# Optimization experiments

Measured on AMD Instinct MI355X. Metric: run time of the kernel, lower is better.

The kernel has to match this reference:

```python
import jax, jax.numpy as jnp
import numpy as np

R = 8          # shuffle_rate
HEADS = 4
DIM_HEAD = 64


def setup_inputs() -> dict:
    key = jax.random.key(0)
    k1, k2, k3 = jax.random.split(key, 3)
    dim = 64
    C = dim * R * R            # 4096, token channel dim after unshuffle
    inner = HEADS * DIM_HEAD   # 256
    x = jax.random.normal(k1, (8, dim, 256, 256), dtype=jnp.float32)
    W_qkv = jax.random.normal(k2, (C, 3 * inner), dtype=jnp.float32) * (C ** -0.5)
    W_out = jax.random.normal(k3, (inner, C), dtype=jnp.float32) * (inner ** -0.5)
    b_out = jnp.zeros((C,), dtype=jnp.float32)
    return {"x": x, "W_qkv": W_qkv, "W_out": W_out, "b_out": b_out}


def reference(x, W_qkv, W_out, b_out):
    scale = DIM_HEAD ** -0.5
    B, C0, H0, W0 = x.shape
    h, w = H0 // R, W0 // R
    N = h * w
    C = C0 * R * R
    # PixelUnshuffle: [B,C0,H0,W0] -> [B, C0*R*R, h, w]
    xd = x.reshape(B, C0, h, R, w, R).transpose(0, 1, 3, 5, 2, 4).reshape(B, C, h, w)
    # flatten spatial -> tokens [B, N, C]
    tokens = xd.reshape(B, C, N).transpose(0, 2, 1)
    qkv = tokens @ W_qkv                                   # [B, N, 3*inner]
    q, k, v = jnp.split(qkv, 3, axis=-1)
    def heads(t):  # [B,N,inner] -> [B,H,N,d]
        return t.reshape(B, N, HEADS, DIM_HEAD).transpose(0, 2, 1, 3)
    q, k, v = heads(q), heads(k), heads(v)
    dots = jnp.einsum('bhnd,bhmd->bhnm', q, k) * scale
    attn = jax.nn.softmax(dots, axis=-1)
    out = jnp.einsum('bhnm,bhmd->bhnd', attn, v)
    out = out.transpose(0, 2, 1, 3).reshape(B, N, HEADS * DIM_HEAD)
    y = out @ W_out + b_out                                # [B, N, C]
    y = y.transpose(0, 2, 1).reshape(B, C, h, w)
    # PixelShuffle: [B, C0*R*R, h, w] -> [B, C0, H0, W0]
    y = y.reshape(B, C0, R, R, h, w).transpose(0, 1, 4, 2, 5, 3).reshape(B, C0, H0, W0)
    return y
```

## Files before the change

kernel.cpp:

```cpp
#include <hip/hip_runtime.h>

typedef unsigned short u16;
typedef __attribute__((ext_vector_type(8))) short s16x8;
typedef __attribute__((ext_vector_type(4))) short s16x4;
typedef __attribute__((ext_vector_type(4))) float f32x4;

__device__ __forceinline__ u16 f2bf(float f) {
    unsigned int u;
    __builtin_memcpy(&u, &f, 4);
    unsigned int r = u + 0x7FFFu + ((u >> 16) & 1u);
    return (u16)(r >> 16);
}

__device__ __forceinline__ unsigned int cvt_pk_bf16(float a, float b) {
    unsigned int r;
    asm("v_cvt_pk_bf16_f32 %0, %1, %2" : "=v"(r) : "v"(a), "v"(b));
    return r;
}

__device__ __forceinline__ void gl_lds16(const u16* g, u16* l) {
    __builtin_amdgcn_global_load_lds(
        (const __attribute__((address_space(1))) unsigned int*)g,
        (__attribute__((address_space(3))) unsigned int*)l,
        16, 0, 0);
}

__global__ __launch_bounds__(256) void k_transpose(const float* __restrict__ in,
                                                   u16* __restrict__ out,
                                                   int rows, int cols) {
    __shared__ float tile[64][65];
    int bx = blockIdx.x * 64, by = blockIdx.y * 64;
    int tx = threadIdx.x & 63, ty = threadIdx.x >> 6;
    for (int i = ty; i < 64; i += 4)
        tile[i][tx] = in[(size_t)(by + i) * cols + bx + tx];
    __syncthreads();
    for (int i = ty; i < 64; i += 4)
        out[(size_t)(bx + i) * rows + by + tx] = f2bf(tile[tx][i]);
}

__global__ __launch_bounds__(512, 1) void k_gemm_qkv(const float* __restrict__ x,
                                                     const u16* __restrict__ Bt,
                                                     float* __restrict__ P) {
    const int K = 4096;
    __shared__ u16 As[256 * 64];
    __shared__ u16 Bs[256 * 64];
    const int tid = threadIdx.x;
    const int wave = tid >> 6, lane = tid & 63;
    const int quad = lane >> 4, l15 = lane & 15;
    const int wm = wave >> 2, wn = wave & 3;

    int lin = blockIdx.x;
    int rem = (lin & 7) * 48 + (lin >> 3);
    int tn3 = rem % 3;
    int q   = rem / 3;
    int z   = q >> 5;
    int tmi = q & 31;
    const int tm = tmi * 256, tn = tn3 * 256;

    const int b   = tm >> 10;
    const int yy0 = (tm & 1023) >> 5;
    const float* asrc = x + ((size_t)(b * 64 + z * 16)) * 65536
                          + yy0 * 2048 + tid * 4;

    u16* dstA[8];
#pragma unroll
    for (int seg = 0; seg < 8; ++seg) {
        int xx  = (tid >> 1) & 31;
        int row = seg * 32 + xx;
        int k2  = wave * 16 + (tid & 1) * 8;
        int byteoff = (row * 128 + k2) ^ ((row & 7) << 4);
        dstA[seg] = (u16*)((char*)As + byteoff);
    }

    float4 va[8];
#pragma unroll
    for (int seg = 0; seg < 8; ++seg)
        va[seg] = *(const float4*)(asrc + seg * 2048);

    f32x4 acc[8][4] = {};

    for (int it = 0; it < 16; ++it) {
        int k0 = z * 1024 + it * 64;
        __syncthreads();
#pragma unroll
        for (int qq = 0; qq < 4; ++qq) {
            int chunk = qq * 512 + tid;
            int row = chunk >> 3, kc = chunk & 7;
            gl_lds16(Bt + (size_t)(tn + row) * K + k0 + kc * 8,
                     Bs + chunk * 8);
        }
#pragma unroll
        for (int seg = 0; seg < 8; ++seg) {
            uint2 pk;
            pk.x = cvt_pk_bf16(va[seg].x, va[seg].y);
            pk.y = cvt_pk_bf16(va[seg].z, va[seg].w);
            *(uint2*)dstA[seg] = pk;
        }
        __syncthreads();
        if (it < 15) {
            asrc += 65536;
#pragma unroll
            for (int seg = 0; seg < 8; ++seg)
                va[seg] = *(const float4*)(asrc + seg * 2048);
        }
        for (int kk = 0; kk < 64; kk += 32) {
            s16x8 af[8], bf[4];
#pragma unroll
            for (int i = 0; i < 8; ++i) {
                int row = wm * 128 + i * 16 + l15;
                int byteoff = (row * 128 + kk * 2 + quad * 16) ^ ((l15 & 7) << 4);
                af[i] = *(const s16x8*)((const char*)As + byteoff);
            }
#pragma unroll
            for (int j = 0; j < 4; ++j)
                bf[j] = *(const s16x8*)(Bs + (wn * 64 + j * 16 + l15) * 64 + kk + quad * 8);
#pragma unroll
            for (int i = 0; i < 8; ++i)
#pragma unroll
                for (int j = 0; j < 4; ++j)
                    acc[i][j] = __builtin_amdgcn_mfma_f32_16x16x32_bf16(af[i], bf[j], acc[i][j], 0, 0, 0);
        }
    }

    float* Pz = P + (size_t)z * 8192 * 768;
    for (int i = 0; i < 8; ++i) {
        int mb = tm + wm * 128 + i * 16 + quad * 4;
        for (int j = 0; j < 4; ++j) {
            int col = tn + wn * 64 + j * 16 + l15;
            for (int r = 0; r < 4; ++r)
                Pz[(size_t)(mb + r) * 768 + col] = acc[i][j][r];
        }
    }
}

__global__ __launch_bounds__(256) void k_qkv_reduce(const float* __restrict__ P,
                                                    u16* __restrict__ Qo,
                                                    u16* __restrict__ Ko,
                                                    u16* __restrict__ Vt) {
    __shared__ u16 tile[64][65];
    const int tid = threadIdx.x;
    const int ct = blockIdx.x, mt = blockIdx.y;
    const int c_l = tid & 63;
    const int col = ct * 64 + c_l;
    const int mbase = mt * 64;
    const size_t NP = (size_t)8192 * 768;
    const float* P1 = P + NP;
    const float* P2 = P + 2 * NP;
    const float* P3 = P + 3 * NP;

    if (ct < 8) {
        int which = col >> 8;
        int h = (col >> 6) & 3, d = col & 63;
        u16* dst = (which == 0) ? Qo : Ko;
        for (int k = 0; k < 16; ++k) {
            int m = mbase + (tid >> 6) + k * 4;
            size_t off = (size_t)m * 768 + col;
            float v = P[off] + P1[off] + P2[off] + P3[off];
            int b = m >> 10, n = m & 1023;
            dst[((size_t)((b * 4 + h) * 1024 + n)) * 64 + d] = f2bf(v);
        }
    } else {
        int h = ct - 8;
        int b = mbase >> 10;
        int nbase = mbase & 1023;
        for (int k = 0; k < 16; ++k) {
            int ml = (tid >> 6) + k * 4;
            int m = mbase + ml;
            size_t off = (size_t)m * 768 + col;
            float v = P[off] + P1[off] + P2[off] + P3[off];
            tile[ml][c_l] = f2bf(v);
        }
        __syncthreads();
        for (int k = 0; k < 16; ++k) {
            int d = (tid >> 6) + k * 4;
            Vt[((size_t)((b * 4 + h) * 64 + d)) * 1024 + nbase + c_l] = tile[c_l][d];
        }
    }
}

__global__ __launch_bounds__(256) void k_attn(const u16* __restrict__ Qb,
                                              const u16* __restrict__ Kb,
                                              const u16* __restrict__ Vt,
                                              u16* __restrict__ aout) {
    const int bh = blockIdx.y;
    const int q0 = blockIdx.x * 64;
    const int tid = threadIdx.x;
    const int wave = tid >> 6, lane = tid & 63;
    const int quad = lane >> 4, l15 = lane & 15;
    const size_t base = (size_t)bh * 1024 * 64;
    const float scale = 0.125f;

    __shared__ u16 Ks[64 * 64];
    __shared__ u16 Vts[64 * 68];
    __shared__ u16 Ps[4][16 * 64];

    s16x8 aq0, aq1;
    {
        const u16* qp = Qb + base + (size_t)(q0 + wave * 16 + l15) * 64 + quad * 8;
        aq0 = *(const s16x8*)(qp);
        aq1 = *(const s16x8*)(qp + 32);
    }

    float m_i[4], l_i[4];
    f32x4 o[4] = {};
    for (int r = 0; r < 4; ++r) { m_i[r] = -1e30f; l_i[r] = 0.f; }

    const int vrow = tid >> 2, vpart = tid & 3;

    for (int t = 0; t < 16; ++t) {
        __syncthreads();
        for (int e = 0; e < 2; ++e) {
            int s = e * 256 + tid;
            gl_lds16(Kb + base + (size_t)t * 4096 + s * 8, Ks + s * 8);
        }
        {
            const u16* src = Vt + base + (size_t)vrow * 1024 + t * 64 + vpart * 16;
            s16x8 a = *(const s16x8*)(src);
            s16x8 b2 = *(const s16x8*)(src + 8);
            *(s16x8*)(Vts + vrow * 68 + vpart * 16) = a;
            *(s16x8*)(Vts + vrow * 68 + vpart * 16 + 8) = b2;
        }
        __syncthreads();

        f32x4 s4[4];
        for (int j = 0; j < 4; ++j) {
            const u16* kr = Ks + (j * 16 + l15) * 64 + quad * 8;
            s16x8 b0 = *(const s16x8*)(kr);
            s16x8 b1 = *(const s16x8*)(kr + 32);
            f32x4 c = {};
            c = __builtin_amdgcn_mfma_f32_16x16x32_bf16(aq0, b0, c, 0, 0, 0);
            c = __builtin_amdgcn_mfma_f32_16x16x32_bf16(aq1, b1, c, 0, 0, 0);
            s4[j] = c;
        }

        for (int r = 0; r < 4; ++r) {
            float sv0 = s4[0][r] * scale, sv1 = s4[1][r] * scale;
            float sv2 = s4[2][r] * scale, sv3 = s4[3][r] * scale;
            float mt = fmaxf(fmaxf(sv0, sv1), fmaxf(sv2, sv3));
            for (int off = 1; off < 16; off <<= 1)
                mt = fmaxf(mt, __shfl_xor(mt, off, 64));
            float mn = fmaxf(m_i[r], mt);
            float alpha = __expf(m_i[r] - mn);
            m_i[r] = mn;
            float p0 = __expf(sv0 - mn), p1 = __expf(sv1 - mn);
            float p2 = __expf(sv2 - mn), p3 = __expf(sv3 - mn);
            u16* pw = Ps[wave] + (quad * 4 + r) * 64 + l15;
            pw[0]  = f2bf(p0);
            pw[16] = f2bf(p1);
            pw[32] = f2bf(p2);
            pw[48] = f2bf(p3);
            float rs = p0 + p1 + p2 + p3;
            for (int off = 1; off < 16; off <<= 1)
                rs += __shfl_xor(rs, off, 64);
            l_i[r] = l_i[r] * alpha + rs;
            for (int dt = 0; dt < 4; ++dt) o[dt][r] *= alpha;
        }

        for (int kk = 0; kk < 64; kk += 32) {
            s16x8 pf = *(const s16x8*)(Ps[wave] + l15 * 64 + kk + quad * 8);
            for (int dt = 0; dt < 4; ++dt) {
                const u16* vr = Vts + (dt * 16 + l15) * 68 + kk + quad * 8;
                s16x4 v0 = *(const s16x4*)(vr);
                s16x4 v1 = *(const s16x4*)(vr + 4);
                s16x8 vf;
                vf[0] = v0[0]; vf[1] = v0[1]; vf[2] = v0[2]; vf[3] = v0[3];
                vf[4] = v1[0]; vf[5] = v1[1]; vf[6] = v1[2]; vf[7] = v1[3];
                o[dt] = __builtin_amdgcn_mfma_f32_16x16x32_bf16(pf, vf, o[dt], 0, 0, 0);
            }
        }
    }

    int b = bh >> 2, h = bh & 3;
    float rl[4];
    for (int r = 0; r < 4; ++r) rl[r] = 1.0f / l_i[r];
    for (int dt = 0; dt < 4; ++dt)
        for (int r = 0; r < 4; ++r) {
            int qrow = q0 + wave * 16 + quad * 4 + r;
            aout[((size_t)(b) * 1024 + qrow) * 256 + h * 64 + dt * 16 + l15] =
                f2bf(o[dt][r] * rl[r]);
        }
}

__global__ __launch_bounds__(256) void k_gemm_out(const u16* __restrict__ A,
                                                  const u16* __restrict__ Bt,
                                                  const float* __restrict__ bias,
                                                  float* __restrict__ out) {
    const int K = 256;
    __shared__ u16 As[128 * 64];
    __shared__ u16 Bs[128 * 64];
    const int tid = threadIdx.x;
    const int wave = tid >> 6, lane = tid & 63;
    const int quad = lane >> 4, l15 = lane & 15;
    const int wm = wave >> 1, wn = wave & 1;
    const int tm = blockIdx.y * 128, tn = blockIdx.x * 128;

    f32x4 acc[4][4] = {};

    for (int k0 = 0; k0 < K; k0 += 64) {
        __syncthreads();
        for (int t = 0; t < 4; ++t) {
            int c = wave * 256 + t * 64 + lane;
            int row = c >> 3, kc = c & 7;
            gl_lds16(A + (size_t)(tm + row) * K + k0 + kc * 8,
                     As + (wave * 256 + t * 64) * 8);
        }
        for (int t = 0; t < 4; ++t) {
            int c = wave * 256 + t * 64 + lane;
            int row = c >> 3, kc = c & 7;
            gl_lds16(Bt + (size_t)(tn + row) * K + k0 + kc * 8,
                     Bs + (wave * 256 + t * 64) * 8);
        }
        __syncthreads();
        for (int kk = 0; kk < 64; kk += 32) {
            s16x8 af[4], bf[4];
            for (int i = 0; i < 4; ++i)
                af[i] = *(const s16x8*)(As + (wm * 64 + i * 16 + l15) * 64 + kk + quad * 8);
            for (int j = 0; j < 4; ++j)
                bf[j] = *(const s16x8*)(Bs + (wn * 64 + j * 16 + l15) * 64 + kk + quad * 8);
            for (int i = 0; i < 4; ++i)
                for (int j = 0; j < 4; ++j)
                    acc[i][j] = __builtin_amdgcn_mfma_f32_16x16x32_bf16(af[i], bf[j], acc[i][j], 0, 0, 0);
        }
    }

    for (int i = 0; i < 4; ++i) {
        int mb = tm + wm * 64 + i * 16 + quad * 4;
        for (int j = 0; j < 4; ++j) {
            int col = tn + wn * 64 + j * 16 + l15;
            float bb = bias[col];
            int c0 = col >> 6, r1 = (col >> 3) & 7, r2 = col & 7;
            for (int r = 0; r < 4; ++r) {
                int m = mb + r;
                int b = m >> 10, n = m & 1023, yy = n >> 5, xx = n & 31;
                size_t oidx = ((size_t)((b * 64 + c0) * 256 + yy * 8 + r1)) * 256 + xx * 8 + r2;
                out[oidx] = acc[i][j][r] + bb;
            }
        }
    }
}

extern "C" void kernel_launch(void* const* d_in, const int* in_sizes, int n_in,
                              void* d_out, int out_size, void* d_ws, size_t ws_size,
                              hipStream_t stream) {
    (void)in_sizes; (void)n_in; (void)out_size; (void)ws_size;
    const float* x    = (const float*)d_in[0];
    const float* Wqkv = (const float*)d_in[1];
    const float* Wout = (const float*)d_in[2];
    const float* bout = (const float*)d_in[3];
    float* out = (float*)d_out;

    u16* ws     = (u16*)d_ws;
    u16* wqkvT  = ws;
    u16* woutT  = wqkvT + 3145728;
    u16* Qb     = woutT + 1048576;
    u16* Kb     = Qb + 2097152;
    u16* Vtb    = Kb + 2097152;
    u16* aoutb  = Vtb + 2097152;
    float* Pp   = (float*)(aoutb + 2097152);

    k_transpose<<<dim3(12, 64), 256, 0, stream>>>(Wqkv, wqkvT, 4096, 768);
    k_transpose<<<dim3(64, 4), 256, 0, stream>>>(Wout, woutT, 256, 4096);
    k_gemm_qkv<<<dim3(384, 1, 1), 512, 0, stream>>>(x, wqkvT, Pp);
    k_qkv_reduce<<<dim3(12, 128), 256, 0, stream>>>(Pp, Qb, Kb, Vtb);
    k_attn<<<dim3(16, 32), 256, 0, stream>>>(Qb, Kb, Vtb, aoutb);
    k_gemm_out<<<dim3(32, 64), 256, 0, stream>>>(aoutb, woutT, bout, out);
}
```

Measured before the change: 413.3 us.

## Double-buffer QKV GEMM LDS tiles with BK=32 and pre-swizzled weight layout

Restructures the QKV projection GEMM main loop into a double-buffered pipeline with a K-step of 32. The next B tile is fetched via global_load_lds and the converted A tile is written into the alternate buffer while MFMAs run on the current one, so only one barrier is needed per step. The weight transpose now writes an XOR-swizzled K layout so direct-to-LDS loads land bank-conflict-free. MFMA sections are wrapped in s_setprio. The cost is twice as many loop iterations and barriers, plus a coupled layout change between the transpose and the GEMM that must stay consistent.

Measured after the change: 397.2 us. -3.9%, faster.

```diff
diff --git a/kernel.cpp b/kernel.cpp
--- a/kernel.cpp
+++ b/kernel.cpp
@@ -27,23 +27,25 @@
 
 __global__ __launch_bounds__(256) void k_transpose(const float* __restrict__ in,
                                                    u16* __restrict__ out,
-                                                   int rows, int cols) {
+                                                   int rows, int cols, int swz) {
     __shared__ float tile[64][65];
     int bx = blockIdx.x * 64, by = blockIdx.y * 64;
     int tx = threadIdx.x & 63, ty = threadIdx.x >> 6;
     for (int i = ty; i < 64; i += 4)
         tile[i][tx] = in[(size_t)(by + i) * cols + bx + tx];
     __syncthreads();
-    for (int i = ty; i < 64; i += 4)
-        out[(size_t)(bx + i) * rows + by + tx] = f2bf(tile[tx][i]);
+    for (int i = ty; i < 64; i += 4) {
+        int n = bx + i, k = by + tx;
+        int ks = swz ? (k ^ (((n >> 1) & 3) << 3)) : k;
+        out[(size_t)n * rows + ks] = f2bf(tile[tx][i]);
+    }
 }
 
 __global__ __launch_bounds__(512, 1) void k_gemm_qkv(const float* __restrict__ x,
                                                      const u16* __restrict__ Bt,
                                                      float* __restrict__ P) {
-    const int K = 4096;
-    __shared__ u16 As[256 * 64];
-    __shared__ u16 Bs[256 * 64];
+    __shared__ u16 As[2][256 * 32];
+    __shared__ u16 Bs[2][256 * 32];
     const int tid = threadIdx.x;
     const int wave = tid >> 6, lane = tid & 63;
     const int quad = lane >> 4, l15 = lane & 15;
@@ -52,74 +54,111 @@
     int lin = blockIdx.x;
     int rem = (lin & 7) * 48 + (lin >> 3);
     int tn3 = rem % 3;
-    int q   = rem / 3;
-    int z   = q >> 5;
-    int tmi = q & 31;
+    int q2  = rem / 3;
+    int z   = q2 >> 5;
+    int tmi = q2 & 31;
     const int tm = tmi * 256, tn = tn3 * 256;
 
     const int b   = tm >> 10;
     const int yy0 = (tm & 1023) >> 5;
-    const float* asrc = x + ((size_t)(b * 64 + z * 16)) * 65536
-                          + yy0 * 2048 + tid * 4;
-
-    u16* dstA[8];
-#pragma unroll
-    for (int seg = 0; seg < 8; ++seg) {
-        int xx  = (tid >> 1) & 31;
-        int row = seg * 32 + xx;
-        int k2  = wave * 16 + (tid & 1) * 8;
-        int byteoff = (row * 128 + k2) ^ ((row & 7) << 4);
-        dstA[seg] = (u16*)((char*)As + byteoff);
-    }
-
-    float4 va[8];
-#pragma unroll
-    for (int seg = 0; seg < 8; ++seg)
-        va[seg] = *(const float4*)(asrc + seg * 2048);
+
+    const int rr    = tid >> 4;
+    const int col16 = tid & 15;
+    const int yy_l  = rr >> 2, r1_l = rr & 3;
+    const int m0    = yy_l * 32 + col16 * 2;
+
+    u16* dstA0[2]; u16* dstA1[2];
+#pragma unroll
+    for (int bb = 0; bb < 2; ++bb) {
+        int off0 = (m0 * 64 + r1_l * 16) ^ (((m0 >> 1) & 3) << 4);
+        int off1 = ((m0 + 1) * 64 + r1_l * 16) ^ ((((m0 + 1) >> 1) & 3) << 4);
+        dstA0[bb] = (u16*)((char*)As[bb] + off0);
+        dstA1[bb] = (u16*)((char*)As[bb] + off1);
+    }
+    const float* planeBase = x + ((size_t)(b * 64)) * 65536
+                               + ((yy0 + yy_l) * 8 + r1_l) * 256 + col16 * 16;
+
+    const int brow = tid >> 2, bo = (tid & 3) * 16;
+    const char* btb = (const char*)Bt;
 
     f32x4 acc[8][4] = {};
-
-    for (int it = 0; it < 16; ++it) {
-        int k0 = z * 1024 + it * 64;
-        __syncthreads();
-#pragma unroll
-        for (int qq = 0; qq < 4; ++qq) {
-            int chunk = qq * 512 + tid;
-            int row = chunk >> 3, kc = chunk & 7;
-            gl_lds16(Bt + (size_t)(tn + row) * K + k0 + kc * 8,
-                     Bs + chunk * 8);
-        }
-#pragma unroll
-        for (int seg = 0; seg < 8; ++seg) {
-            uint2 pk;
-            pk.x = cvt_pk_bf16(va[seg].x, va[seg].y);
-            pk.y = cvt_pk_bf16(va[seg].z, va[seg].w);
-            *(uint2*)dstA[seg] = pk;
-        }
-        __syncthreads();
-        if (it < 15) {
-            asrc += 65536;
-#pragma unroll
-            for (int seg = 0; seg < 8; ++seg)
-                va[seg] = *(const float4*)(asrc + seg * 2048);
-        }
-        for (int kk = 0; kk < 64; kk += 32) {
-            s16x8 af[8], bf[4];
-#pragma unroll
-            for (int i = 0; i < 8; ++i) {
-                int row = wm * 128 + i * 16 + l15;
-                int byteoff = (row * 128 + kk * 2 + quad * 16) ^ ((l15 & 7) << 4);
-                af[i] = *(const s16x8*)((const char*)As + byteoff);
-            }
+    float4 va[4];
+
+    {
+        const float* s = planeBase;
+        s += (size_t)(z * 16) * 65536;
+#pragma unroll
+        for (int j = 0; j < 4; ++j) va[j] = ((const float4*)s)[j];
+    }
+    {
+        size_t koff = (size_t)z * 2048;
+        gl_lds16((const u16*)(btb + (size_t)(tn + brow) * 8192 + koff + bo),
+                 Bs[0] + tid * 8);
+        gl_lds16((const u16*)(btb + (size_t)(tn + 128 + brow) * 8192 + koff + bo),
+                 Bs[0] + 4096 + tid * 8);
+    }
+    {
+        uint4 pk0, pk1;
+        pk0.x = cvt_pk_bf16(va[0].x, va[0].y); pk0.y = cvt_pk_bf16(va[0].z, va[0].w);
+        pk0.z = cvt_pk_bf16(va[1].x, va[1].y); pk0.w = cvt_pk_bf16(va[1].z, va[1].w);
+        pk1.x = cvt_pk_bf16(va[2].x, va[2].y); pk1.y = cvt_pk_bf16(va[2].z, va[2].w);
+        pk1.z = cvt_pk_bf16(va[3].x, va[3].y); pk1.w = cvt_pk_bf16(va[3].z, va[3].w);
+        *(uint4*)dstA0[0] = pk0;
+        *(uint4*)dstA1[0] = pk1;
+    }
+    {
+        const float* s = planeBase + (size_t)(z * 16) * 65536 + 1024;
+#pragma unroll
+        for (int j = 0; j < 4; ++j) va[j] = ((const float4*)s)[j];
+    }
+    __syncthreads();
+
+    int cur = 0;
+    for (int it = 0; it < 32; ++it) {
+        if (it < 31) {
+            int it1 = it + 1;
+            size_t koff = (size_t)z * 2048 + (size_t)it1 * 64;
+            gl_lds16((const u16*)(btb + (size_t)(tn + brow) * 8192 + koff + bo),
+                     Bs[cur ^ 1] + tid * 8);
+            gl_lds16((const u16*)(btb + (size_t)(tn + 128 + brow) * 8192 + koff + bo),
+                     Bs[cur ^ 1] + 4096 + tid * 8);
+            uint4 pk0, pk1;
+            pk0.x = cvt_pk_bf16(va[0].x, va[0].y); pk0.y = cvt_pk_bf16(va[0].z, va[0].w);
+            pk0.z = cvt_pk_bf16(va[1].x, va[1].y); pk0.w = cvt_pk_bf16(va[1].z, va[1].w);
+            pk1.x = cvt_pk_bf16(va[2].x, va[2].y); pk1.y = cvt_pk_bf16(va[2].z, va[2].w);
+            pk1.z = cvt_pk_bf16(va[3].x, va[3].y); pk1.w = cvt_pk_bf16(va[3].z, va[3].w);
+            *(uint4*)dstA0[cur ^ 1] = pk0;
+            *(uint4*)dstA1[cur ^ 1] = pk1;
+        }
+        if (it < 30) {
+            int it2 = it + 2;
+            const float* s = planeBase + (size_t)(z * 16 + (it2 >> 1)) * 65536
+                           + (it2 & 1) * 1024;
+#pragma unroll
+            for (int j = 0; j < 4; ++j) va[j] = ((const float4*)s)[j];
+        }
+        s16x8 af[8], bf[4];
+#pragma unroll
+        for (int i = 0; i < 8; ++i) {
+            int row = wm * 128 + i * 16 + l15;
+            int off = (row * 64 + quad * 16) ^ (((row >> 1) & 3) << 4);
+            af[i] = *(const s16x8*)((const char*)As[cur] + off);
+        }
+#pragma unroll
+        for (int j = 0; j < 4; ++j) {
+            int row = wn * 64 + j * 16 + l15;
+            int off = (row * 64 + quad * 16) ^ (((row >> 1) & 3) << 4);
+            bf[j] = *(const s16x8*)((const char*)Bs[cur] + off);
+        }
+        __builtin_amdgcn_s_setprio(1);
+#pragma unroll
+        for (int i = 0; i < 8; ++i)
 #pragma unroll
             for (int j = 0; j < 4; ++j)
-                bf[j] = *(const s16x8*)(Bs + (wn * 64 + j * 16 + l15) * 64 + kk + quad * 8);
-#pragma unroll
-            for (int i = 0; i < 8; ++i)
-#pragma unroll
-                for (int j = 0; j < 4; ++j)
-                    acc[i][j] = __builtin_amdgcn_mfma_f32_16x16x32_bf16(af[i], bf[j], acc[i][j], 0, 0, 0);
-        }
+                acc[i][j] = __builtin_amdgcn_mfma_f32_16x16x32_bf16(af[i], bf[j], acc[i][j], 0, 0, 0);
+        __builtin_amdgcn_s_setprio(0);
+        __syncthreads();
+        cur ^= 1;
     }
 
     float* Pz = P + (size_t)z * 8192 * 768;
@@ -358,8 +397,8 @@
     u16* aoutb  = Vtb + 2097152;
     float* Pp   = (float*)(aoutb + 2097152);
 
-    k_transpose<<<dim3(12, 64), 256, 0, stream>>>(Wqkv, wqkvT, 4096, 768);
-    k_transpose<<<dim3(64, 4), 256, 0, stream>>>(Wout, woutT, 256, 4096);
+    k_transpose<<<dim3(12, 64), 256, 0, stream>>>(Wqkv, wqkvT, 4096, 768, 1);
+    k_transpose<<<dim3(64, 4), 256, 0, stream>>>(Wout, woutT, 256, 4096, 0);
     k_gemm_qkv<<<dim3(384, 1, 1), 512, 0, stream>>>(x, wqkvT, Pp);
     k_qkv_reduce<<<dim3(12, 128), 256, 0, stream>>>(Pp, Qb, Kb, Vtb);
     k_attn<<<dim3(16, 32), 256, 0, stream>>>(Qb, Kb, Vtb, aoutb);
```
